# Performance work log

Measured on AMD Instinct MI355X. Metric: run time of the kernel, lower is better.

## Reference

```python
import jax, jax.numpy as jnp
import numpy as np

INPUT_SIZE = 64
HIDDEN_SIZE = 256
NUM_CLASSES = 10
BATCH = 512
SEQ_LEN = 1024


def setup_inputs() -> dict:
    key = jax.random.key(0)
    ks = jax.random.split(key, 6)
    std = 1.0 / np.sqrt(HIDDEN_SIZE)
    x = jax.random.normal(ks[0], (BATCH, SEQ_LEN, INPUT_SIZE), dtype=jnp.float32)
    # GRUCell params (reset_parameters: uniform(-std, std))
    Wx = jax.random.uniform(ks[1], (3 * HIDDEN_SIZE, INPUT_SIZE), minval=-std, maxval=std, dtype=jnp.float32)
    Wh = jax.random.uniform(ks[2], (3 * HIDDEN_SIZE, HIDDEN_SIZE), minval=-std, maxval=std, dtype=jnp.float32)
    bias = jax.random.uniform(ks[3], (3 * HIDDEN_SIZE,), minval=-std, maxval=std, dtype=jnp.float32)
    # fc: Linear(hidden_size, num_classes), default torch init ~ uniform(-1/sqrt(H), 1/sqrt(H))
    fc_w = jax.random.uniform(ks[4], (NUM_CLASSES, HIDDEN_SIZE), minval=-std, maxval=std, dtype=jnp.float32)
    fc_b = jax.random.uniform(ks[5], (NUM_CLASSES,), minval=-std, maxval=std, dtype=jnp.float32)
    return {"x": x, "Wx": Wx, "Wh": Wh, "bias": bias, "fc_w": fc_w, "fc_b": fc_b}


def reference(x, Wx, Wh, bias, fc_w, fc_b):
    B, S, _ = x.shape
    H = Wh.shape[1]
    b_r, b_z, b_h = jnp.split(bias, 3)
    # Precompute input gates for all timesteps in one GEMM: [B, S, 3H]
    gate_x = jnp.einsum('bsi,gi->bsg', x, Wx)

    def step(h, gx_t):
        gate_h = h @ Wh.T  # [B, 3H]
        i_r, i_z, i_h = jnp.split(gx_t, 3, axis=1)
        h_r, h_z, h_h = jnp.split(gate_h, 3, axis=1)
        reset_gate = jax.nn.sigmoid(i_r + h_r + b_r)
        update_gate = jax.nn.sigmoid(i_z + h_z + b_z)
        new_gate = jnp.tanh(i_h + reset_gate * h_h + b_h)
        hy = new_gate + update_gate * (h - new_gate)
        return hy, None

    h0 = jnp.zeros((B, H), dtype=x.dtype)
    hT, _ = jax.lax.scan(step, h0, jnp.swapaxes(gate_x, 0, 1))  # scan over time
    logit = hT @ fc_w.T + fc_b
    return logit
```

## Files before the change

kernel.cpp:

```cpp
#include <hip/hip_runtime.h>
#include <hip/hip_fp16.h>


typedef short v8s __attribute__((ext_vector_type(8)));
typedef float f32x4 __attribute__((ext_vector_type(4)));

#define LOG2E 1.4426950408889634f
#define GX_ELEMS (512ull * 1024ull * 768ull)
#define WS_NEED (GX_ELEMS * 2ull)

__device__ __forceinline__ unsigned short f2b(float f) {
    unsigned int u = __float_as_uint(f);
    u += 0x7FFFu + ((u >> 16) & 1u);
    return (unsigned short)(u >> 16);
}
__device__ __forceinline__ float b2f(unsigned short h) {
    return __uint_as_float(((unsigned int)h) << 16);
}
__device__ __forceinline__ v8s cvt8(f32x4 a, f32x4 b) {
    v8s r;
#pragma unroll
    for (int j = 0; j < 4; ++j) { r[j] = (short)f2b(a[j]); r[4 + j] = (short)f2b(b[j]); }
    return r;
}
__device__ __forceinline__ v8s wfrag(const float* src, float s) {
    f32x4 a = *(const f32x4*)src, b = *(const f32x4*)(src + 4);
    a *= s; b *= s;
    return cvt8(a, b);
}
__device__ __forceinline__ float rcpf(float v) {
#if __has_builtin(__builtin_amdgcn_rcpf)
    return __builtin_amdgcn_rcpf(v);
#else
    return 1.0f / v;
#endif
}
__device__ __forceinline__ float exp2f_(float v) {
#if __has_builtin(__builtin_amdgcn_exp2f)
    return __builtin_amdgcn_exp2f(v);
#else
    return __exp2f(v);
#endif
}
__device__ __forceinline__ float sg(float v) { return rcpf(1.0f + exp2f_(-v)); }
__device__ __forceinline__ float sigm(float v) {
    float e = __expf(-fmaxf(v, -30.0f));
    return rcpf(1.0f + e);
}
__device__ __forceinline__ float tanh_(float v) {
    float vc = fmaxf(fminf(v, 30.0f), -30.0f);
    float e = __expf(-2.0f * vc);
    return (1.0f - e) * rcpf(1.0f + e);
}
__device__ __forceinline__ f32x4 MF(v8s a, v8s b, f32x4 c) {
    return __builtin_amdgcn_mfma_f32_16x16x32_bf16(a, b, c, 0, 0, 0);
}
__device__ __forceinline__ int fidx(int row, int k) {
    return ((k >> 5) << 9) + ((((k >> 3) & 3) << 4) + row) * 8 + (k & 7);
}

extern "C" __global__ void __launch_bounds__(512)
gx_prepass(const float* __restrict__ x, const float* __restrict__ Wx,
           const float* __restrict__ bias, __half* __restrict__ gx)
{
    extern __shared__ char plds[];
    v8s* wxf = (v8s*)plds;

    const int tid = threadIdx.x;
    const int w = tid >> 6, l = tid & 63;
    const int cl = l & 15, kg = l >> 4;
    const int g = blockIdx.x & 31, tc = blockIdx.x >> 5;
    const int b0 = g << 4;

    for (int fid = w; fid < 96; fid += 8) {
        int ct = fid >> 1, k2 = fid & 1;
        float sc = (ct < 32) ? LOG2E : 2.0f * LOG2E;
        const float* src = Wx + (size_t)(ct * 16 + cl) * 64 + k2 * 32 + kg * 8;
        wxf[fid * 64 + l] = wfrag(src, sc);
    }
    __syncthreads();

    const int tiles[6] = {2*w, 2*w+1, 16+2*w, 17+2*w, 32+2*w, 33+2*w};
    float bv[6];
#pragma unroll
    for (int tt = 0; tt < 6; ++tt)
        bv[tt] = bias[tiles[tt] * 16 + cl] * ((tt < 4) ? LOG2E : 2.0f * LOG2E);

    for (int t16 = 0; t16 < 16; ++t16) {
        const int t = tc * 16 + t16;
        const float* xs = x + ((size_t)(b0 + cl) * 1024 + t) * 64 + kg * 8;
        v8s a0 = cvt8(*(const f32x4*)xs,        *(const f32x4*)(xs + 4));
        v8s a1 = cvt8(*(const f32x4*)(xs + 32), *(const f32x4*)(xs + 36));

        f32x4 acc[6];
#pragma unroll
        for (int tt = 0; tt < 6; ++tt) {
            acc[tt] = f32x4{0, 0, 0, 0};
            acc[tt] = MF(a0, wxf[(tiles[tt] * 2) * 64 + l], acc[tt]);
            acc[tt] = MF(a1, wxf[(tiles[tt] * 2 + 1) * 64 + l], acc[tt]);
        }
        const size_t rbase = (size_t)t * 512 + b0 + (kg << 2);
#pragma unroll
        for (int tt = 0; tt < 6; ++tt)
#pragma unroll
            for (int i = 0; i < 4; ++i)
                gx[(rbase + i) * 768 + tiles[tt] * 16 + cl] =
                    __float2half_rn(acc[tt][i] + bv[tt]);
    }
}

#define S_LDS_WHN  0
#define S_LDS_H    131072
#define S_LDS_SIZE 147456

extern "C" __global__ void __launch_bounds__(512, 2)
gru_scan2(const float* __restrict__ Wh, const __half* __restrict__ gx,
          const float* __restrict__ fcw, const float* __restrict__ fcb,
          float* __restrict__ out)
{
    extern __shared__ char lds[];
    v8s* whn = (v8s*)(lds + S_LDS_WHN);
    char* hl = lds + S_LDS_H;

    const int tid = threadIdx.x;
    const int w = tid >> 6, l = tid & 63;
    const int cl = l & 15, kg = l >> 4;
    const int b0 = blockIdx.x << 4;

    for (int f = w; f < 128; f += 8) {
        int t5 = f >> 3, ks = f & 7;
        const float* src = Wh + (size_t)(512 + t5 * 16 + cl) * 256 + ks * 32 + kg * 8;
        whn[f * 64 + l] = wfrag(src, 2.0f * LOG2E);
    }
    v8s whB[4][8];
#pragma unroll
    for (int tt = 0; tt < 4; ++tt) {
        const int tv = (tt < 2) ? (2 * w + tt) : (16 + 2 * w + (tt - 2));
        const float* src = Wh + (size_t)(tv * 16 + cl) * 256 + kg * 8;
#pragma unroll
        for (int ks = 0; ks < 8; ++ks)
            whB[tt][ks] = wfrag(src + ks * 32, LOG2E);
    }

    for (int i = tid; i < 2048; i += 512) ((unsigned int*)hl)[i] = 0u;
    float hprev[8] = {0, 0, 0, 0, 0, 0, 0, 0};
    const int wn0 = (2 * w) * 8, wn1 = (2 * w + 1) * 8;
    const __half* gq = gx + (size_t)(b0 + (kg << 2)) * 768 + w * 32 + cl;

    for (int t = 0; t < 1024; ++t) {
        __syncthreads();
        const int cur = t & 1;
        const v8s* hb = (const v8s*)(hl + cur * 8192);

        __half gxv[24];
#pragma unroll
        for (int gate = 0; gate < 3; ++gate)
#pragma unroll
            for (int p = 0; p < 2; ++p)
#pragma unroll
                for (int i = 0; i < 4; ++i)
                    gxv[gate * 8 + p * 4 + i] = gq[gate * 256 + p * 16 + i * 768];
        gq += 393216;

        f32x4 aR[2] = {{0,0,0,0},{0,0,0,0}}, aZ[2] = {{0,0,0,0},{0,0,0,0}},
              aN[2] = {{0,0,0,0},{0,0,0,0}};
#pragma unroll
        for (int ks = 0; ks < 8; ++ks) {
            v8s a  = hb[(ks << 6) + l];
            v8s n0 = whn[(wn0 + ks) * 64 + l];
            v8s n1 = whn[(wn1 + ks) * 64 + l];
            aR[0] = MF(a, whB[0][ks], aR[0]);
            aR[1] = MF(a, whB[1][ks], aR[1]);
            aZ[0] = MF(a, whB[2][ks], aZ[0]);
            aZ[1] = MF(a, whB[3][ks], aZ[1]);
            aN[0] = MF(a, n0, aN[0]);
            aN[1] = MF(a, n1, aN[1]);
        }

        unsigned short* hn = (unsigned short*)(hl + (cur ^ 1) * 8192);
#pragma unroll
        for (int p = 0; p < 2; ++p) {
            const int ch = w * 32 + p * 16 + cl;
            const int chbase = ((ch >> 5) << 9) + (((ch >> 3) & 3) << 7) + (ch & 7);
#pragma unroll
            for (int i = 0; i < 4; ++i) {
                float rg = sg(aR[p][i] + __half2float(gxv[p * 4 + i]));
                float zg = sg(aZ[p][i] + __half2float(gxv[8 + p * 4 + i]));
                float nv = __builtin_fmaf(rg, aN[p][i], __half2float(gxv[16 + p * 4 + i]));
                float ng = __builtin_fmaf(2.0f, sg(nv), -1.0f);
                float hy = ng + zg * (hprev[p * 4 + i] - ng);
                hprev[p * 4 + i] = hy;
                hn[chbase + ((kg << 2) + i) * 8] = f2b(hy);
            }
        }
    }

    __syncthreads();
    const unsigned short* hf = (const unsigned short*)hl;
    if (tid < 160) {
        int row = tid / 10, cls = tid - row * 10;
        float s = fcb[cls];
        const float* wrow = fcw + cls * 256;
        for (int k = 0; k < 256; ++k)
            s += b2f(hf[fidx(row, k)]) * wrow[k];
        out[(b0 + row) * 10 + cls] = s;
    }
}

#define FB_LDS_SIZE 151552
extern "C" __global__ void __launch_bounds__(512, 2)
gru_fb(const float* __restrict__ x, const float* __restrict__ Wx,
       const float* __restrict__ Wh, const float* __restrict__ bias,
       const float* __restrict__ fcw, const float* __restrict__ fcb,
       float* __restrict__ out)
{
    extern __shared__ char lds[];
    v8s* whn = (v8s*)lds;
    char* hl = lds + 131072;
    char* xl = lds + 147456;
    const int tid = threadIdx.x;
    const int w = tid >> 6, l = tid & 63;
    const int cl = l & 15, kg = l >> 4;
    const int b0 = blockIdx.x << 4;
    const int tiles[6] = {2*w, 2*w+1, 16+2*w, 17+2*w, 32+2*w, 33+2*w};

    for (int f = w; f < 128; f += 8) {
        int t5 = f >> 3, ks = f & 7;
        const float* src = Wh + (size_t)(512 + t5*16 + cl)*256 + ks*32 + kg*8;
        whn[f*64 + l] = wfrag(src, 1.0f);
    }
    v8s whB[4][8];
#pragma unroll
    for (int tt = 0; tt < 4; ++tt) {
        const float* src = Wh + (size_t)(tiles[tt]*16 + cl)*256 + kg*8;
#pragma unroll
        for (int ks = 0; ks < 8; ++ks)
            whB[tt][ks] = wfrag(src + ks*32, 1.0f);
    }
    float brv[2], bzv[2], bhv[2];
#pragma unroll
    for (int p = 0; p < 2; ++p) {
        int ch = (w << 5) + (p << 4) + cl;
        brv[p] = bias[ch]; bzv[p] = bias[256+ch]; bhv[p] = bias[512+ch];
    }
    for (int i = tid; i < 2048; i += 512) ((unsigned int*)hl)[i] = 0u;
    const int xr = tid >> 5, xc = (tid & 31) << 1;
    const int xidx = fidx(xr, xc);
    const float* xp = x + (((size_t)(b0 + xr)) << 16) + xc;
    {
        unsigned int pk = (unsigned int)f2b(xp[0]) | ((unsigned int)f2b(xp[1]) << 16);
        *(unsigned int*)(xl + xidx*2) = pk;
    }
    xp += 64;
    const int wn0 = (2*w)*8, wn1 = (2*w+1)*8;

    for (int t = 0; t < 1024; ++t) {
        __syncthreads();
        const int cur = t & 1;
        const v8s* hb = (const v8s*)(hl + cur*8192);
        const v8s* xb = (const v8s*)(xl + cur*2048);
        float xv0 = 0.0f, xv1 = 0.0f;
        if (t < 1023) { xv0 = xp[0]; xv1 = xp[1]; xp += 64; }
        v8s wxr[12];
#pragma unroll
        for (int tt = 0; tt < 6; ++tt) {
            const float* s0 = Wx + (size_t)(tiles[tt]*16 + cl)*64 + kg*8;
            wxr[tt*2]   = wfrag(s0, 1.0f);
            wxr[tt*2+1] = wfrag(s0 + 32, 1.0f);
        }
        f32x4 acc[8];
#pragma unroll
        for (int i = 0; i < 8; ++i) acc[i] = f32x4{0,0,0,0};
#pragma unroll
        for (int ks = 0; ks < 8; ++ks) {
            v8s a = hb[(ks << 6) + l];
            v8s n0 = whn[(wn0 + ks)*64 + l];
            v8s n1 = whn[(wn1 + ks)*64 + l];
            acc[0] = MF(a, whB[0][ks], acc[0]);
            acc[1] = MF(a, whB[1][ks], acc[1]);
            acc[2] = MF(a, whB[2][ks], acc[2]);
            acc[3] = MF(a, whB[3][ks], acc[3]);
            acc[4] = MF(a, n0, acc[4]);
            acc[5] = MF(a, n1, acc[5]);
        }
#pragma unroll
        for (int k2 = 0; k2 < 2; ++k2) {
            v8s ax = xb[(k2 << 6) + l];
            acc[0] = MF(ax, wxr[0+k2], acc[0]);
            acc[1] = MF(ax, wxr[2+k2], acc[1]);
            acc[2] = MF(ax, wxr[4+k2], acc[2]);
            acc[3] = MF(ax, wxr[6+k2], acc[3]);
            acc[6] = MF(ax, wxr[8+k2], acc[6]);
            acc[7] = MF(ax, wxr[10+k2], acc[7]);
        }
        const unsigned short* hc16 = (const unsigned short*)hb;
        unsigned short* hn16 = (unsigned short*)(hl + ((cur ^ 1) * 8192));
#pragma unroll
        for (int p = 0; p < 2; ++p) {
            int ch = (w << 5) + (p << 4) + cl;
            int chbase = ((ch >> 5) << 9) + (((ch >> 3) & 3) << 7) + (ch & 7);
#pragma unroll
            for (int i = 0; i < 4; ++i) {
                int row = (kg << 2) + i;
                int idx = chbase + (row << 3);
                float rg = sigm(acc[p][i] + brv[p]);
                float zg = sigm(acc[2+p][i] + bzv[p]);
                float ng = tanh_(acc[6+p][i] + bhv[p] + rg * acc[4+p][i]);
                float hold = b2f(hc16[idx]);
                float hy = ng + zg * (hold - ng);
                hn16[idx] = f2b(hy);
            }
        }
        if (t < 1023) {
            unsigned int pk = (unsigned int)f2b(xv0) | ((unsigned int)f2b(xv1) << 16);
            *(unsigned int*)(xl + ((cur ^ 1) * 2048) + xidx*2) = pk;
        }
    }
    __syncthreads();
    const unsigned short* hf = (const unsigned short*)hl;
    if (tid < 160) {
        int row = tid / 10, cls = tid - row * 10;
        float s = fcb[cls];
        const float* wrow = fcw + cls * 256;
        for (int k = 0; k < 256; ++k)
            s += b2f(hf[fidx(row, k)]) * wrow[k];
        out[(b0 + row)*10 + cls] = s;
    }
}

extern "C" void kernel_launch(void* const* d_in, const int* in_sizes, int n_in,
                              void* d_out, int out_size, void* d_ws, size_t ws_size,
                              hipStream_t stream) {
    const float* x    = (const float*)d_in[0];
    const float* Wx   = (const float*)d_in[1];
    const float* Wh   = (const float*)d_in[2];
    const float* bias = (const float*)d_in[3];
    const float* fcw  = (const float*)d_in[4];
    const float* fcb  = (const float*)d_in[5];

    if (ws_size >= WS_NEED) {
        (void)hipFuncSetAttribute((const void*)gx_prepass,
                                  hipFuncAttributeMaxDynamicSharedMemorySize, 98304);
        (void)hipFuncSetAttribute((const void*)gru_scan2,
                                  hipFuncAttributeMaxDynamicSharedMemorySize, S_LDS_SIZE);
        gx_prepass<<<dim3(2048), dim3(512), 98304, stream>>>(
            x, Wx, bias, (__half*)d_ws);
        gru_scan2<<<dim3(32), dim3(512), S_LDS_SIZE, stream>>>(
            Wh, (const __half*)d_ws, fcw, fcb, (float*)d_out);
    } else {
        (void)hipFuncSetAttribute((const void*)gru_fb,
                                  hipFuncAttributeMaxDynamicSharedMemorySize, FB_LDS_SIZE);
        gru_fb<<<dim3(32), dim3(512), FB_LDS_SIZE, stream>>>(
            x, Wx, Wh, bias, fcw, fcb, (float*)d_out);
    }
}
```

Before: 2.029 ms.

## Fuse input-gate prepass into scan kernel with producer-consumer chunked ring buffer

```diff
diff --git a/kernel.cpp b/kernel.cpp
--- a/kernel.cpp
+++ b/kernel.cpp
@@ -4,10 +4,9 @@
 
 typedef short v8s __attribute__((ext_vector_type(8)));
 typedef float f32x4 __attribute__((ext_vector_type(4)));
+typedef unsigned short u16x4 __attribute__((ext_vector_type(4)));
 
 #define LOG2E 1.4426950408889634f
-#define GX_ELEMS (512ull * 1024ull * 768ull)
-#define WS_NEED (GX_ELEMS * 2ull)
 
 __device__ __forceinline__ unsigned short f2b(float f) {
     unsigned int u = __float_as_uint(f);
@@ -16,6 +15,16 @@
 }
 __device__ __forceinline__ float b2f(unsigned short h) {
     return __uint_as_float(((unsigned int)h) << 16);
+}
+__device__ __forceinline__ unsigned short f2h(float f) {
+    union { __half h; unsigned short u; } cv;
+    cv.h = __float2half_rn(f);
+    return cv.u;
+}
+__device__ __forceinline__ float h2f(unsigned short u) {
+    union { unsigned short u; __half h; } cv;
+    cv.u = u;
+    return __half2float(cv.h);
 }
 __device__ __forceinline__ v8s cvt8(f32x4 a, f32x4 b) {
     v8s r;
@@ -59,73 +68,93 @@
     return ((k >> 5) << 9) + ((((k >> 3) & 3) << 4) + row) * 8 + (k & 7);
 }
 
-extern "C" __global__ void __launch_bounds__(512)
-gx_prepass(const float* __restrict__ x, const float* __restrict__ Wx,
-           const float* __restrict__ bias, __half* __restrict__ gx)
+#define S_LDS_SIZE 147456
+
+extern "C" __global__ void __launch_bounds__(512, 2)
+gru_fused(const float* __restrict__ x, const float* __restrict__ Wx,
+          const float* __restrict__ Wh, const float* __restrict__ bias,
+          const float* __restrict__ fcw, const float* __restrict__ fcb,
+          unsigned short* __restrict__ gx, unsigned int* __restrict__ ctrl,
+          int n_slots, int ch_shift, float* __restrict__ out)
 {
-    extern __shared__ char plds[];
-    v8s* wxf = (v8s*)plds;
-
+    extern __shared__ char lds[];
     const int tid = threadIdx.x;
     const int w = tid >> 6, l = tid & 63;
     const int cl = l & 15, kg = l >> 4;
-    const int g = blockIdx.x & 31, tc = blockIdx.x >> 5;
-    const int b0 = g << 4;
-
-    for (int fid = w; fid < 96; fid += 8) {
-        int ct = fid >> 1, k2 = fid & 1;
-        float sc = (ct < 32) ? LOG2E : 2.0f * LOG2E;
-        const float* src = Wx + (size_t)(ct * 16 + cl) * 64 + k2 * 32 + kg * 8;
-        wxf[fid * 64 + l] = wfrag(src, sc);
-    }
-    __syncthreads();
-
-    const int tiles[6] = {2*w, 2*w+1, 16+2*w, 17+2*w, 32+2*w, 33+2*w};
-    float bv[6];
-#pragma unroll
-    for (int tt = 0; tt < 6; ++tt)
-        bv[tt] = bias[tiles[tt] * 16 + cl] * ((tt < 4) ? LOG2E : 2.0f * LOG2E);
-
-    for (int t16 = 0; t16 < 16; ++t16) {
-        const int t = tc * 16 + t16;
-        const float* xs = x + ((size_t)(b0 + cl) * 1024 + t) * 64 + kg * 8;
-        v8s a0 = cvt8(*(const f32x4*)xs,        *(const f32x4*)(xs + 4));
-        v8s a1 = cvt8(*(const f32x4*)(xs + 32), *(const f32x4*)(xs + 36));
-
-        f32x4 acc[6];
-#pragma unroll
-        for (int tt = 0; tt < 6; ++tt) {
-            acc[tt] = f32x4{0, 0, 0, 0};
-            acc[tt] = MF(a0, wxf[(tiles[tt] * 2) * 64 + l], acc[tt]);
-            acc[tt] = MF(a1, wxf[(tiles[tt] * 2 + 1) * 64 + l], acc[tt]);
-        }
-        const size_t rbase = (size_t)t * 512 + b0 + (kg << 2);
+    const size_t slot_elems = 393216ull << ch_shift;
+
+    if (blockIdx.x >= 32) {
+        v8s* wxf = (v8s*)lds;
+        const int pid = blockIdx.x - 32;
+        const int cs4 = ch_shift - 4;
+
+        for (int fid = w; fid < 96; fid += 8) {
+            int ct = fid >> 1, k2 = fid & 1;
+            float sc = (ct < 32) ? LOG2E : 2.0f * LOG2E;
+            const float* src = Wx + (size_t)(ct * 16 + cl) * 64 + k2 * 32 + kg * 8;
+            wxf[fid * 64 + l] = wfrag(src, sc);
+        }
+        const int tiles[6] = {2*w, 2*w+1, 16+2*w, 17+2*w, 32+2*w, 33+2*w};
+        float bv[6];
 #pragma unroll
         for (int tt = 0; tt < 6; ++tt)
-#pragma unroll
-            for (int i = 0; i < 4; ++i)
-                gx[(rbase + i) * 768 + tiles[tt] * 16 + cl] =
-                    __float2half_rn(acc[tt][i] + bv[tt]);
-    }
-}
-
-#define S_LDS_WHN  0
-#define S_LDS_H    131072
-#define S_LDS_SIZE 147456
-
-extern "C" __global__ void __launch_bounds__(512, 2)
-gru_scan2(const float* __restrict__ Wh, const __half* __restrict__ gx,
-          const float* __restrict__ fcw, const float* __restrict__ fcb,
-          float* __restrict__ out)
-{
-    extern __shared__ char lds[];
-    v8s* whn = (v8s*)(lds + S_LDS_WHN);
-    char* hl = lds + S_LDS_H;
-
-    const int tid = threadIdx.x;
-    const int w = tid >> 6, l = tid & 63;
-    const int cl = l & 15, kg = l >> 4;
+            bv[tt] = bias[tiles[tt] * 16 + cl] * ((tt < 4) ? LOG2E : 2.0f * LOG2E);
+        __syncthreads();
+
+        for (int j = pid; j < 2048; j += 224) {
+            const int tc = j >> 5, g = j & 31;
+            const int c = tc >> cs4;
+            const int b0 = g << 4;
+            if (c >= n_slots) {
+                if (tid == 0) {
+                    while (__hip_atomic_load(&ctrl[64 + (c - n_slots)],
+                                             __ATOMIC_ACQUIRE,
+                                             __HIP_MEMORY_SCOPE_AGENT) < 32u)
+                        __builtin_amdgcn_s_sleep(16);
+                }
+                __syncthreads();
+            }
+            unsigned short* gs = gx + (size_t)(c % n_slots) * slot_elems;
+            const int tl0 = (tc << 4) - (c << ch_shift);
+
+            for (int t16 = 0; t16 < 16; ++t16) {
+                const int t = (tc << 4) + t16;
+                const int tl = tl0 + t16;
+                const float* xs = x + ((size_t)(b0 + cl) * 1024 + t) * 64 + kg * 8;
+                v8s a0 = cvt8(*(const f32x4*)xs,        *(const f32x4*)(xs + 4));
+                v8s a1 = cvt8(*(const f32x4*)(xs + 32), *(const f32x4*)(xs + 36));
+
+                f32x4 acc[6];
+#pragma unroll
+                for (int tt = 0; tt < 6; ++tt) {
+                    acc[tt] = f32x4{0, 0, 0, 0};
+                    acc[tt] = MF(a0, wxf[(tiles[tt] * 2) * 64 + l], acc[tt]);
+                    acc[tt] = MF(a1, wxf[(tiles[tt] * 2 + 1) * 64 + l], acc[tt]);
+                }
+#pragma unroll
+                for (int tt = 0; tt < 6; ++tt) {
+                    u16x4 pk;
+#pragma unroll
+                    for (int i = 0; i < 4; ++i)
+                        pk[i] = f2h(acc[tt][i] + bv[tt]);
+                    *(u16x4*)(gs + (size_t)(tl * 768 + tiles[tt] * 16 + cl) * 512
+                                 + b0 + (kg << 2)) = pk;
+                }
+            }
+            __syncthreads();
+            if (tid == 0)
+                __hip_atomic_fetch_add(&ctrl[c], 1u, __ATOMIC_RELEASE,
+                                       __HIP_MEMORY_SCOPE_AGENT);
+        }
+        return;
+    }
+
+    v8s* whn = (v8s*)lds;
+    char* hl = lds + 131072;
     const int b0 = blockIdx.x << 4;
+    const int nchunk = 1024 >> ch_shift;
+    const int chs = 1 << ch_shift;
+    const unsigned int jobs_pc = 32u << (ch_shift - 4);
 
     for (int f = w; f < 128; f += 8) {
         int t5 = f >> 3, ks = f & 7;
@@ -141,58 +170,69 @@
         for (int ks = 0; ks < 8; ++ks)
             whB[tt][ks] = wfrag(src + ks * 32, LOG2E);
     }
-
     for (int i = tid; i < 2048; i += 512) ((unsigned int*)hl)[i] = 0u;
     float hprev[8] = {0, 0, 0, 0, 0, 0, 0, 0};
     const int wn0 = (2 * w) * 8, wn1 = (2 * w + 1) * 8;
-    const __half* gq = gx + (size_t)(b0 + (kg << 2)) * 768 + w * 32 + cl;
-
-    for (int t = 0; t < 1024; ++t) {
+    const size_t gxoff = (size_t)((w << 5) + cl) * 512 + b0 + (kg << 2);
+
+    int t = 0;
+    for (int c = 0; c < nchunk; ++c) {
+        if (tid == 0) {
+            while (__hip_atomic_load(&ctrl[c], __ATOMIC_ACQUIRE,
+                                     __HIP_MEMORY_SCOPE_AGENT) < jobs_pc)
+                __builtin_amdgcn_s_sleep(16);
+        }
+        const unsigned short* gp = gx + (size_t)(c % n_slots) * slot_elems + gxoff;
+
+        for (int t2 = 0; t2 < chs; ++t2, ++t) {
+            __syncthreads();
+            const int cur = t & 1;
+            const v8s* hb = (const v8s*)(hl + cur * 8192);
+
+            u16x4 gv[6];
+#pragma unroll
+            for (int gi = 0; gi < 3; ++gi)
+#pragma unroll
+                for (int p = 0; p < 2; ++p)
+                    gv[gi * 2 + p] = *(const u16x4*)(gp + (size_t)(gi * 256 + p * 16) * 512);
+            gp += 393216;
+
+            f32x4 aR[2] = {{0,0,0,0},{0,0,0,0}}, aZ[2] = {{0,0,0,0},{0,0,0,0}},
+                  aN[2] = {{0,0,0,0},{0,0,0,0}};
+#pragma unroll
+            for (int ks = 0; ks < 8; ++ks) {
+                v8s a  = hb[(ks << 6) + l];
+                v8s n0 = whn[(wn0 + ks) * 64 + l];
+                v8s n1 = whn[(wn1 + ks) * 64 + l];
+                aR[0] = MF(a, whB[0][ks], aR[0]);
+                aR[1] = MF(a, whB[1][ks], aR[1]);
+                aZ[0] = MF(a, whB[2][ks], aZ[0]);
+                aZ[1] = MF(a, whB[3][ks], aZ[1]);
+                aN[0] = MF(a, n0, aN[0]);
+                aN[1] = MF(a, n1, aN[1]);
+            }
+
+            unsigned short* hn = (unsigned short*)(hl + (cur ^ 1) * 8192);
+#pragma unroll
+            for (int p = 0; p < 2; ++p) {
+                const int ch = (w << 5) + (p << 4) + cl;
+                const int chbase = ((ch >> 5) << 9) + (((ch >> 3) & 3) << 7) + (ch & 7);
+#pragma unroll
+                for (int i = 0; i < 4; ++i) {
+                    float rg = sg(aR[p][i] + h2f(gv[p][i]));
+                    float zg = sg(aZ[p][i] + h2f(gv[2 + p][i]));
+                    float nv = __builtin_fmaf(rg, aN[p][i], h2f(gv[4 + p][i]));
+                    float ng = __builtin_fmaf(2.0f, sg(nv), -1.0f);
+                    float hy = ng + zg * (hprev[p * 4 + i] - ng);
+                    hprev[p * 4 + i] = hy;
+                    hn[chbase + ((kg << 2) + i) * 8] = f2b(hy);
+                }
+            }
+        }
         __syncthreads();
-        const int cur = t & 1;
-        const v8s* hb = (const v8s*)(hl + cur * 8192);
-
-        __half gxv[24];
-#pragma unroll
-        for (int gate = 0; gate < 3; ++gate)
-#pragma unroll
-            for (int p = 0; p < 2; ++p)
-#pragma unroll
-                for (int i = 0; i < 4; ++i)
-                    gxv[gate * 8 + p * 4 + i] = gq[gate * 256 + p * 16 + i * 768];
-        gq += 393216;
-
-        f32x4 aR[2] = {{0,0,0,0},{0,0,0,0}}, aZ[2] = {{0,0,0,0},{0,0,0,0}},
-              aN[2] = {{0,0,0,0},{0,0,0,0}};
-#pragma unroll
-        for (int ks = 0; ks < 8; ++ks) {
-            v8s a  = hb[(ks << 6) + l];
-            v8s n0 = whn[(wn0 + ks) * 64 + l];
-            v8s n1 = whn[(wn1 + ks) * 64 + l];
-            aR[0] = MF(a, whB[0][ks], aR[0]);
-            aR[1] = MF(a, whB[1][ks], aR[1]);
-            aZ[0] = MF(a, whB[2][ks], aZ[0]);
-            aZ[1] = MF(a, whB[3][ks], aZ[1]);
-            aN[0] = MF(a, n0, aN[0]);
-            aN[1] = MF(a, n1, aN[1]);
-        }
-
-        unsigned short* hn = (unsigned short*)(hl + (cur ^ 1) * 8192);
-#pragma unroll
-        for (int p = 0; p < 2; ++p) {
-            const int ch = w * 32 + p * 16 + cl;
-            const int chbase = ((ch >> 5) << 9) + (((ch >> 3) & 3) << 7) + (ch & 7);
-#pragma unroll
-            for (int i = 0; i < 4; ++i) {
-                float rg = sg(aR[p][i] + __half2float(gxv[p * 4 + i]));
-                float zg = sg(aZ[p][i] + __half2float(gxv[8 + p * 4 + i]));
-                float nv = __builtin_fmaf(rg, aN[p][i], __half2float(gxv[16 + p * 4 + i]));
-                float ng = __builtin_fmaf(2.0f, sg(nv), -1.0f);
-                float hy = ng + zg * (hprev[p * 4 + i] - ng);
-                hprev[p * 4 + i] = hy;
-                hn[chbase + ((kg << 2) + i) * 8] = f2b(hy);
-            }
-        }
+        if (tid == 0)
+            __hip_atomic_fetch_add(&ctrl[64 + c], 1u, __ATOMIC_RELEASE,
+                                   __HIP_MEMORY_SCOPE_AGENT);
     }
 
     __syncthreads();
@@ -338,15 +378,26 @@
     const float* fcw  = (const float*)d_in[4];
     const float* fcb  = (const float*)d_in[5];
 
-    if (ws_size >= WS_NEED) {
-        (void)hipFuncSetAttribute((const void*)gx_prepass,
-                                  hipFuncAttributeMaxDynamicSharedMemorySize, 98304);
-        (void)hipFuncSetAttribute((const void*)gru_scan2,
+    int ch_shift = -1, n_slots = 0;
+    for (int cs = 6; cs >= 4; --cs) {
+        unsigned long long slot = 786432ull << cs;
+        if (ws_size < 1024ull + 2ull * slot) continue;
+        int nch = 1024 >> cs;
+        unsigned long long n = (ws_size - 1024ull) / slot;
+        n_slots = (n > (unsigned long long)nch) ? nch : (int)n;
+        ch_shift = cs;
+        break;
+    }
+
+    if (ch_shift >= 4) {
+        unsigned int* ctrl =
+            (unsigned int*)((char*)d_ws + (786432ull << ch_shift) * (size_t)n_slots);
+        (void)hipMemsetAsync(ctrl, 0, 1024, stream);
+        (void)hipFuncSetAttribute((const void*)gru_fused,
                                   hipFuncAttributeMaxDynamicSharedMemorySize, S_LDS_SIZE);
-        gx_prepass<<<dim3(2048), dim3(512), 98304, stream>>>(
-            x, Wx, bias, (__half*)d_ws);
-        gru_scan2<<<dim3(32), dim3(512), S_LDS_SIZE, stream>>>(
-            Wh, (const __half*)d_ws, fcw, fcb, (float*)d_out);
+        gru_fused<<<dim3(256), dim3(512), S_LDS_SIZE, stream>>>(
+            x, Wx, Wh, bias, fcw, fcb,
+            (unsigned short*)d_ws, ctrl, n_slots, ch_shift, (float*)d_out);
     } else {
         (void)hipFuncSetAttribute((const void*)gru_fb,
                                   hipFuncAttributeMaxDynamicSharedMemorySize, FB_LDS_SIZE);
```

After: 6.118 ms. 3.01x slower.

## Fuse input projection into recurrent scan and drop the gx prepass

Applied to the files above, without the earlier changes.

```diff
diff --git a/kernel.cpp b/kernel.cpp
--- a/kernel.cpp
+++ b/kernel.cpp
@@ -1,13 +1,10 @@
 #include <hip/hip_runtime.h>
-#include <hip/hip_fp16.h>
 
 
 typedef short v8s __attribute__((ext_vector_type(8)));
 typedef float f32x4 __attribute__((ext_vector_type(4)));
 
 #define LOG2E 1.4426950408889634f
-#define GX_ELEMS (512ull * 1024ull * 768ull)
-#define WS_NEED (GX_ELEMS * 2ull)
 
 __device__ __forceinline__ unsigned short f2b(float f) {
     unsigned int u = __float_as_uint(f);
@@ -43,15 +40,6 @@
 #endif
 }
 __device__ __forceinline__ float sg(float v) { return rcpf(1.0f + exp2f_(-v)); }
-__device__ __forceinline__ float sigm(float v) {
-    float e = __expf(-fmaxf(v, -30.0f));
-    return rcpf(1.0f + e);
-}
-__device__ __forceinline__ float tanh_(float v) {
-    float vc = fmaxf(fminf(v, 30.0f), -30.0f);
-    float e = __expf(-2.0f * vc);
-    return (1.0f - e) * rcpf(1.0f + e);
-}
 __device__ __forceinline__ f32x4 MF(v8s a, v8s b, f32x4 c) {
     return __builtin_amdgcn_mfma_f32_16x16x32_bf16(a, b, c, 0, 0, 0);
 }
@@ -59,165 +47,21 @@
     return ((k >> 5) << 9) + ((((k >> 3) & 3) << 4) + row) * 8 + (k & 7);
 }
 
-extern "C" __global__ void __launch_bounds__(512)
-gx_prepass(const float* __restrict__ x, const float* __restrict__ Wx,
-           const float* __restrict__ bias, __half* __restrict__ gx)
-{
-    extern __shared__ char plds[];
-    v8s* wxf = (v8s*)plds;
-
-    const int tid = threadIdx.x;
-    const int w = tid >> 6, l = tid & 63;
-    const int cl = l & 15, kg = l >> 4;
-    const int g = blockIdx.x & 31, tc = blockIdx.x >> 5;
-    const int b0 = g << 4;
-
-    for (int fid = w; fid < 96; fid += 8) {
-        int ct = fid >> 1, k2 = fid & 1;
-        float sc = (ct < 32) ? LOG2E : 2.0f * LOG2E;
-        const float* src = Wx + (size_t)(ct * 16 + cl) * 64 + k2 * 32 + kg * 8;
-        wxf[fid * 64 + l] = wfrag(src, sc);
-    }
-    __syncthreads();
-
-    const int tiles[6] = {2*w, 2*w+1, 16+2*w, 17+2*w, 32+2*w, 33+2*w};
-    float bv[6];
-#pragma unroll
-    for (int tt = 0; tt < 6; ++tt)
-        bv[tt] = bias[tiles[tt] * 16 + cl] * ((tt < 4) ? LOG2E : 2.0f * LOG2E);
-
-    for (int t16 = 0; t16 < 16; ++t16) {
-        const int t = tc * 16 + t16;
-        const float* xs = x + ((size_t)(b0 + cl) * 1024 + t) * 64 + kg * 8;
-        v8s a0 = cvt8(*(const f32x4*)xs,        *(const f32x4*)(xs + 4));
-        v8s a1 = cvt8(*(const f32x4*)(xs + 32), *(const f32x4*)(xs + 36));
-
-        f32x4 acc[6];
-#pragma unroll
-        for (int tt = 0; tt < 6; ++tt) {
-            acc[tt] = f32x4{0, 0, 0, 0};
-            acc[tt] = MF(a0, wxf[(tiles[tt] * 2) * 64 + l], acc[tt]);
-            acc[tt] = MF(a1, wxf[(tiles[tt] * 2 + 1) * 64 + l], acc[tt]);
-        }
-        const size_t rbase = (size_t)t * 512 + b0 + (kg << 2);
-#pragma unroll
-        for (int tt = 0; tt < 6; ++tt)
-#pragma unroll
-            for (int i = 0; i < 4; ++i)
-                gx[(rbase + i) * 768 + tiles[tt] * 16 + cl] =
-                    __float2half_rn(acc[tt][i] + bv[tt]);
-    }
-}
-
-#define S_LDS_WHN  0
-#define S_LDS_H    131072
-#define S_LDS_SIZE 147456
+#define LDS_H    131072
+#define LDS_X    147456
+#define LDS_SIZE 151552
 
 extern "C" __global__ void __launch_bounds__(512, 2)
-gru_scan2(const float* __restrict__ Wh, const __half* __restrict__ gx,
-          const float* __restrict__ fcw, const float* __restrict__ fcb,
-          float* __restrict__ out)
-{
-    extern __shared__ char lds[];
-    v8s* whn = (v8s*)(lds + S_LDS_WHN);
-    char* hl = lds + S_LDS_H;
-
-    const int tid = threadIdx.x;
-    const int w = tid >> 6, l = tid & 63;
-    const int cl = l & 15, kg = l >> 4;
-    const int b0 = blockIdx.x << 4;
-
-    for (int f = w; f < 128; f += 8) {
-        int t5 = f >> 3, ks = f & 7;
-        const float* src = Wh + (size_t)(512 + t5 * 16 + cl) * 256 + ks * 32 + kg * 8;
-        whn[f * 64 + l] = wfrag(src, 2.0f * LOG2E);
-    }
-    v8s whB[4][8];
-#pragma unroll
-    for (int tt = 0; tt < 4; ++tt) {
-        const int tv = (tt < 2) ? (2 * w + tt) : (16 + 2 * w + (tt - 2));
-        const float* src = Wh + (size_t)(tv * 16 + cl) * 256 + kg * 8;
-#pragma unroll
-        for (int ks = 0; ks < 8; ++ks)
-            whB[tt][ks] = wfrag(src + ks * 32, LOG2E);
-    }
-
-    for (int i = tid; i < 2048; i += 512) ((unsigned int*)hl)[i] = 0u;
-    float hprev[8] = {0, 0, 0, 0, 0, 0, 0, 0};
-    const int wn0 = (2 * w) * 8, wn1 = (2 * w + 1) * 8;
-    const __half* gq = gx + (size_t)(b0 + (kg << 2)) * 768 + w * 32 + cl;
-
-    for (int t = 0; t < 1024; ++t) {
-        __syncthreads();
-        const int cur = t & 1;
-        const v8s* hb = (const v8s*)(hl + cur * 8192);
-
-        __half gxv[24];
-#pragma unroll
-        for (int gate = 0; gate < 3; ++gate)
-#pragma unroll
-            for (int p = 0; p < 2; ++p)
-#pragma unroll
-                for (int i = 0; i < 4; ++i)
-                    gxv[gate * 8 + p * 4 + i] = gq[gate * 256 + p * 16 + i * 768];
-        gq += 393216;
-
-        f32x4 aR[2] = {{0,0,0,0},{0,0,0,0}}, aZ[2] = {{0,0,0,0},{0,0,0,0}},
-              aN[2] = {{0,0,0,0},{0,0,0,0}};
-#pragma unroll
-        for (int ks = 0; ks < 8; ++ks) {
-            v8s a  = hb[(ks << 6) + l];
-            v8s n0 = whn[(wn0 + ks) * 64 + l];
-            v8s n1 = whn[(wn1 + ks) * 64 + l];
-            aR[0] = MF(a, whB[0][ks], aR[0]);
-            aR[1] = MF(a, whB[1][ks], aR[1]);
-            aZ[0] = MF(a, whB[2][ks], aZ[0]);
-            aZ[1] = MF(a, whB[3][ks], aZ[1]);
-            aN[0] = MF(a, n0, aN[0]);
-            aN[1] = MF(a, n1, aN[1]);
-        }
-
-        unsigned short* hn = (unsigned short*)(hl + (cur ^ 1) * 8192);
-#pragma unroll
-        for (int p = 0; p < 2; ++p) {
-            const int ch = w * 32 + p * 16 + cl;
-            const int chbase = ((ch >> 5) << 9) + (((ch >> 3) & 3) << 7) + (ch & 7);
-#pragma unroll
-            for (int i = 0; i < 4; ++i) {
-                float rg = sg(aR[p][i] + __half2float(gxv[p * 4 + i]));
-                float zg = sg(aZ[p][i] + __half2float(gxv[8 + p * 4 + i]));
-                float nv = __builtin_fmaf(rg, aN[p][i], __half2float(gxv[16 + p * 4 + i]));
-                float ng = __builtin_fmaf(2.0f, sg(nv), -1.0f);
-                float hy = ng + zg * (hprev[p * 4 + i] - ng);
-                hprev[p * 4 + i] = hy;
-                hn[chbase + ((kg << 2) + i) * 8] = f2b(hy);
-            }
-        }
-    }
-
-    __syncthreads();
-    const unsigned short* hf = (const unsigned short*)hl;
-    if (tid < 160) {
-        int row = tid / 10, cls = tid - row * 10;
-        float s = fcb[cls];
-        const float* wrow = fcw + cls * 256;
-        for (int k = 0; k < 256; ++k)
-            s += b2f(hf[fidx(row, k)]) * wrow[k];
-        out[(b0 + row) * 10 + cls] = s;
-    }
-}
-
-#define FB_LDS_SIZE 151552
-extern "C" __global__ void __launch_bounds__(512, 2)
-gru_fb(const float* __restrict__ x, const float* __restrict__ Wx,
+gru_v7(const float* __restrict__ x, const float* __restrict__ Wx,
        const float* __restrict__ Wh, const float* __restrict__ bias,
        const float* __restrict__ fcw, const float* __restrict__ fcb,
        float* __restrict__ out)
 {
     extern __shared__ char lds[];
     v8s* whn = (v8s*)lds;
-    char* hl = lds + 131072;
-    char* xl = lds + 147456;
+    char* hl = lds + LDS_H;
+    char* xl = lds + LDS_X;
+
     const int tid = threadIdx.x;
     const int w = tid >> 6, l = tid & 63;
     const int cl = l & 15, kg = l >> 4;
@@ -227,7 +71,7 @@
     for (int f = w; f < 128; f += 8) {
         int t5 = f >> 3, ks = f & 7;
         const float* src = Wh + (size_t)(512 + t5*16 + cl)*256 + ks*32 + kg*8;
-        whn[f*64 + l] = wfrag(src, 1.0f);
+        whn[f*64 + l] = wfrag(src, 2.0f*LOG2E);
     }
     v8s whB[4][8];
 #pragma unroll
@@ -235,15 +79,28 @@
         const float* src = Wh + (size_t)(tiles[tt]*16 + cl)*256 + kg*8;
 #pragma unroll
         for (int ks = 0; ks < 8; ++ks)
-            whB[tt][ks] = wfrag(src + ks*32, 1.0f);
+            whB[tt][ks] = wfrag(src + ks*32, LOG2E);
+    }
+    v8s wxr[12];
+#pragma unroll
+    for (int tt = 0; tt < 6; ++tt) {
+        const float sc = (tt < 4) ? LOG2E : 2.0f*LOG2E;
+        const float* s0 = Wx + (size_t)(tiles[tt]*16 + cl)*64 + kg*8;
+        wxr[tt*2]   = wfrag(s0, sc);
+        wxr[tt*2+1] = wfrag(s0 + 32, sc);
     }
     float brv[2], bzv[2], bhv[2];
 #pragma unroll
     for (int p = 0; p < 2; ++p) {
         int ch = (w << 5) + (p << 4) + cl;
-        brv[p] = bias[ch]; bzv[p] = bias[256+ch]; bhv[p] = bias[512+ch];
-    }
+        brv[p] = bias[ch] * LOG2E;
+        bzv[p] = bias[256 + ch] * LOG2E;
+        bhv[p] = bias[512 + ch] * 2.0f*LOG2E;
+    }
+
     for (int i = tid; i < 2048; i += 512) ((unsigned int*)hl)[i] = 0u;
+    float hprev[8] = {0, 0, 0, 0, 0, 0, 0, 0};
+
     const int xr = tid >> 5, xc = (tid & 31) << 1;
     const int xidx = fidx(xr, xc);
     const float* xp = x + (((size_t)(b0 + xr)) << 16) + xc;
@@ -259,21 +116,23 @@
         const int cur = t & 1;
         const v8s* hb = (const v8s*)(hl + cur*8192);
         const v8s* xb = (const v8s*)(xl + cur*2048);
+
         float xv0 = 0.0f, xv1 = 0.0f;
         if (t < 1023) { xv0 = xp[0]; xv1 = xp[1]; xp += 64; }
-        v8s wxr[12];
-#pragma unroll
-        for (int tt = 0; tt < 6; ++tt) {
-            const float* s0 = Wx + (size_t)(tiles[tt]*16 + cl)*64 + kg*8;
-            wxr[tt*2]   = wfrag(s0, 1.0f);
-            wxr[tt*2+1] = wfrag(s0 + 32, 1.0f);
-        }
+
         f32x4 acc[8];
-#pragma unroll
-        for (int i = 0; i < 8; ++i) acc[i] = f32x4{0,0,0,0};
+        acc[0] = f32x4{brv[0], brv[0], brv[0], brv[0]};
+        acc[1] = f32x4{brv[1], brv[1], brv[1], brv[1]};
+        acc[2] = f32x4{bzv[0], bzv[0], bzv[0], bzv[0]};
+        acc[3] = f32x4{bzv[1], bzv[1], bzv[1], bzv[1]};
+        acc[4] = f32x4{0, 0, 0, 0};
+        acc[5] = f32x4{0, 0, 0, 0};
+        acc[6] = f32x4{bhv[0], bhv[0], bhv[0], bhv[0]};
+        acc[7] = f32x4{bhv[1], bhv[1], bhv[1], bhv[1]};
+
 #pragma unroll
         for (int ks = 0; ks < 8; ++ks) {
-            v8s a = hb[(ks << 6) + l];
+            v8s a  = hb[(ks << 6) + l];
             v8s n0 = whn[(wn0 + ks)*64 + l];
             v8s n1 = whn[(wn1 + ks)*64 + l];
             acc[0] = MF(a, whB[0][ks], acc[0]);
@@ -286,29 +145,28 @@
 #pragma unroll
         for (int k2 = 0; k2 < 2; ++k2) {
             v8s ax = xb[(k2 << 6) + l];
-            acc[0] = MF(ax, wxr[0+k2], acc[0]);
-            acc[1] = MF(ax, wxr[2+k2], acc[1]);
-            acc[2] = MF(ax, wxr[4+k2], acc[2]);
-            acc[3] = MF(ax, wxr[6+k2], acc[3]);
-            acc[6] = MF(ax, wxr[8+k2], acc[6]);
-            acc[7] = MF(ax, wxr[10+k2], acc[7]);
-        }
-        const unsigned short* hc16 = (const unsigned short*)hb;
-        unsigned short* hn16 = (unsigned short*)(hl + ((cur ^ 1) * 8192));
+            acc[0] = MF(ax, wxr[0  + k2], acc[0]);
+            acc[1] = MF(ax, wxr[2  + k2], acc[1]);
+            acc[2] = MF(ax, wxr[4  + k2], acc[2]);
+            acc[3] = MF(ax, wxr[6  + k2], acc[3]);
+            acc[6] = MF(ax, wxr[8  + k2], acc[6]);
+            acc[7] = MF(ax, wxr[10 + k2], acc[7]);
+        }
+
+        unsigned short* hn = (unsigned short*)(hl + (cur ^ 1) * 8192);
 #pragma unroll
         for (int p = 0; p < 2; ++p) {
-            int ch = (w << 5) + (p << 4) + cl;
-            int chbase = ((ch >> 5) << 9) + (((ch >> 3) & 3) << 7) + (ch & 7);
+            const int ch = (w << 5) + (p << 4) + cl;
+            const int chbase = ((ch >> 5) << 9) + (((ch >> 3) & 3) << 7) + (ch & 7);
 #pragma unroll
             for (int i = 0; i < 4; ++i) {
-                int row = (kg << 2) + i;
-                int idx = chbase + (row << 3);
-                float rg = sigm(acc[p][i] + brv[p]);
-                float zg = sigm(acc[2+p][i] + bzv[p]);
-                float ng = tanh_(acc[6+p][i] + bhv[p] + rg * acc[4+p][i]);
-                float hold = b2f(hc16[idx]);
-                float hy = ng + zg * (hold - ng);
-                hn16[idx] = f2b(hy);
+                float rg = sg(acc[p][i]);
+                float zg = sg(acc[2 + p][i]);
+                float nv = __builtin_fmaf(rg, acc[4 + p][i], acc[6 + p][i]);
+                float ng = __builtin_fmaf(2.0f, sg(nv), -1.0f);
+                float hy = ng + zg * (hprev[p*4 + i] - ng);
+                hprev[p*4 + i] = hy;
+                hn[chbase + ((kg << 2) + i) * 8] = f2b(hy);
             }
         }
         if (t < 1023) {
@@ -316,6 +174,7 @@
             *(unsigned int*)(xl + ((cur ^ 1) * 2048) + xidx*2) = pk;
         }
     }
+
     __syncthreads();
     const unsigned short* hf = (const unsigned short*)hl;
     if (tid < 160) {
@@ -337,20 +196,10 @@
     const float* bias = (const float*)d_in[3];
     const float* fcw  = (const float*)d_in[4];
     const float* fcb  = (const float*)d_in[5];
-
-    if (ws_size >= WS_NEED) {
-        (void)hipFuncSetAttribute((const void*)gx_prepass,
-                                  hipFuncAttributeMaxDynamicSharedMemorySize, 98304);
-        (void)hipFuncSetAttribute((const void*)gru_scan2,
-                                  hipFuncAttributeMaxDynamicSharedMemorySize, S_LDS_SIZE);
-        gx_prepass<<<dim3(2048), dim3(512), 98304, stream>>>(
-            x, Wx, bias, (__half*)d_ws);
-        gru_scan2<<<dim3(32), dim3(512), S_LDS_SIZE, stream>>>(
-            Wh, (const __half*)d_ws, fcw, fcb, (float*)d_out);
-    } else {
-        (void)hipFuncSetAttribute((const void*)gru_fb,
-                                  hipFuncAttributeMaxDynamicSharedMemorySize, FB_LDS_SIZE);
-        gru_fb<<<dim3(32), dim3(512), FB_LDS_SIZE, stream>>>(
-            x, Wx, Wh, bias, fcw, fcb, (float*)d_out);
-    }
-}
+    (void)d_ws; (void)ws_size;
+
+    (void)hipFuncSetAttribute((const void*)gru_v7,
+                              hipFuncAttributeMaxDynamicSharedMemorySize, LDS_SIZE);
+    gru_v7<<<dim3(32), dim3(512), LDS_SIZE, stream>>>(
+        x, Wx, Wh, bias, fcw, fcb, (float*)d_out);
+}
```

New measurement: 1.967 ms. -3.1%, faster.

## Fuse input-gate GEMM into scan kernel with per-chunk workspace staging

Applied to the files above, without the earlier changes.

```diff
diff --git a/kernel.cpp b/kernel.cpp
--- a/kernel.cpp
+++ b/kernel.cpp
@@ -4,10 +4,13 @@
 
 typedef short v8s __attribute__((ext_vector_type(8)));
 typedef float f32x4 __attribute__((ext_vector_type(4)));
+typedef unsigned int u32x4 __attribute__((ext_vector_type(4)));
+typedef unsigned int u32x2 __attribute__((ext_vector_type(2)));
 
 #define LOG2E 1.4426950408889634f
-#define GX_ELEMS (512ull * 1024ull * 768ull)
-#define WS_NEED (GX_ELEMS * 2ull)
+#define CHUNK 32
+#define NCHUNK 32
+#define WS_NEED (32ull * CHUNK * 24576ull)
 
 __device__ __forceinline__ unsigned short f2b(float f) {
     unsigned int u = __float_as_uint(f);
@@ -16,6 +19,13 @@
 }
 __device__ __forceinline__ float b2f(unsigned short h) {
     return __uint_as_float(((unsigned int)h) << 16);
+}
+__device__ __forceinline__ unsigned short f2h(float f) {
+    return __half_as_ushort(__float2half_rn(f));
+}
+__device__ __forceinline__ float hxu(unsigned int u, int hi) {
+    unsigned short b = (unsigned short)(hi ? (u >> 16) : (u & 0xFFFFu));
+    return __half2float(__ushort_as_half(b));
 }
 __device__ __forceinline__ v8s cvt8(f32x4 a, f32x4 b) {
     v8s r;
@@ -59,138 +69,153 @@
     return ((k >> 5) << 9) + ((((k >> 3) & 3) << 4) + row) * 8 + (k & 7);
 }
 
-extern "C" __global__ void __launch_bounds__(512)
-gx_prepass(const float* __restrict__ x, const float* __restrict__ Wx,
-           const float* __restrict__ bias, __half* __restrict__ gx)
-{
-    extern __shared__ char plds[];
-    v8s* wxf = (v8s*)plds;
-
-    const int tid = threadIdx.x;
-    const int w = tid >> 6, l = tid & 63;
-    const int cl = l & 15, kg = l >> 4;
-    const int g = blockIdx.x & 31, tc = blockIdx.x >> 5;
-    const int b0 = g << 4;
-
-    for (int fid = w; fid < 96; fid += 8) {
-        int ct = fid >> 1, k2 = fid & 1;
-        float sc = (ct < 32) ? LOG2E : 2.0f * LOG2E;
-        const float* src = Wx + (size_t)(ct * 16 + cl) * 64 + k2 * 32 + kg * 8;
-        wxf[fid * 64 + l] = wfrag(src, sc);
-    }
-    __syncthreads();
-
-    const int tiles[6] = {2*w, 2*w+1, 16+2*w, 17+2*w, 32+2*w, 33+2*w};
-    float bv[6];
-#pragma unroll
-    for (int tt = 0; tt < 6; ++tt)
-        bv[tt] = bias[tiles[tt] * 16 + cl] * ((tt < 4) ? LOG2E : 2.0f * LOG2E);
-
-    for (int t16 = 0; t16 < 16; ++t16) {
-        const int t = tc * 16 + t16;
-        const float* xs = x + ((size_t)(b0 + cl) * 1024 + t) * 64 + kg * 8;
-        v8s a0 = cvt8(*(const f32x4*)xs,        *(const f32x4*)(xs + 4));
-        v8s a1 = cvt8(*(const f32x4*)(xs + 32), *(const f32x4*)(xs + 36));
-
-        f32x4 acc[6];
-#pragma unroll
-        for (int tt = 0; tt < 6; ++tt) {
-            acc[tt] = f32x4{0, 0, 0, 0};
-            acc[tt] = MF(a0, wxf[(tiles[tt] * 2) * 64 + l], acc[tt]);
-            acc[tt] = MF(a1, wxf[(tiles[tt] * 2 + 1) * 64 + l], acc[tt]);
-        }
-        const size_t rbase = (size_t)t * 512 + b0 + (kg << 2);
-#pragma unroll
-        for (int tt = 0; tt < 6; ++tt)
-#pragma unroll
-            for (int i = 0; i < 4; ++i)
-                gx[(rbase + i) * 768 + tiles[tt] * 16 + cl] =
-                    __float2half_rn(acc[tt][i] + bv[tt]);
-    }
-}
-
-#define S_LDS_WHN  0
-#define S_LDS_H    131072
-#define S_LDS_SIZE 147456
+#define LDS8_X    16384
+#define LDS8_SIZE 81920
 
 extern "C" __global__ void __launch_bounds__(512, 2)
-gru_scan2(const float* __restrict__ Wh, const __half* __restrict__ gx,
-          const float* __restrict__ fcw, const float* __restrict__ fcb,
-          float* __restrict__ out)
+gru_v8(const float* __restrict__ x, const float* __restrict__ Wx,
+       const float* __restrict__ Wh, const float* __restrict__ bias,
+       const float* __restrict__ fcw, const float* __restrict__ fcb,
+       unsigned short* __restrict__ ws, float* __restrict__ out)
 {
     extern __shared__ char lds[];
-    v8s* whn = (v8s*)(lds + S_LDS_WHN);
-    char* hl = lds + S_LDS_H;
+    char* hl = lds;
+    char* xf = lds + LDS8_X;
 
     const int tid = threadIdx.x;
     const int w = tid >> 6, l = tid & 63;
     const int cl = l & 15, kg = l >> 4;
     const int b0 = blockIdx.x << 4;
-
-    for (int f = w; f < 128; f += 8) {
-        int t5 = f >> 3, ks = f & 7;
-        const float* src = Wh + (size_t)(512 + t5 * 16 + cl) * 256 + ks * 32 + kg * 8;
-        whn[f * 64 + l] = wfrag(src, 2.0f * LOG2E);
-    }
+    const int tiles[6] = {2*w, 2*w+1, 16+2*w, 17+2*w, 32+2*w, 33+2*w};
+
     v8s whB[4][8];
 #pragma unroll
     for (int tt = 0; tt < 4; ++tt) {
-        const int tv = (tt < 2) ? (2 * w + tt) : (16 + 2 * w + (tt - 2));
-        const float* src = Wh + (size_t)(tv * 16 + cl) * 256 + kg * 8;
+        const float* src = Wh + (size_t)(tiles[tt]*16 + cl)*256 + kg*8;
 #pragma unroll
         for (int ks = 0; ks < 8; ++ks)
-            whB[tt][ks] = wfrag(src + ks * 32, LOG2E);
+            whB[tt][ks] = wfrag(src + ks*32, LOG2E);
     }
 
     for (int i = tid; i < 2048; i += 512) ((unsigned int*)hl)[i] = 0u;
     float hprev[8] = {0, 0, 0, 0, 0, 0, 0, 0};
-    const int wn0 = (2 * w) * 8, wn1 = (2 * w + 1) * 8;
-    const __half* gq = gx + (size_t)(b0 + (kg << 2)) * 768 + w * 32 + cl;
-
-    for (int t = 0; t < 1024; ++t) {
+
+    unsigned short* gxb = ws + (size_t)blockIdx.x * (CHUNK * 12288);
+
+    const int tl_x  = tid >> 4;
+    const int k0    = (tid & 15) << 2;
+    const int k2x   = k0 >> 5;
+    const int laned = ((k0 & 31) >> 3) << 4;
+    const int e2    = (k0 & 7) << 1;
+    char* const xfd = xf + (tl_x*2 + k2x)*1024 + e2;
+
+    for (int c = 0; c < NCHUNK; ++c) {
+        const int c0 = c << 5;
         __syncthreads();
-        const int cur = t & 1;
-        const v8s* hb = (const v8s*)(hl + cur * 8192);
-
-        __half gxv[24];
-#pragma unroll
-        for (int gate = 0; gate < 3; ++gate)
-#pragma unroll
-            for (int p = 0; p < 2; ++p)
-#pragma unroll
-                for (int i = 0; i < 4; ++i)
-                    gxv[gate * 8 + p * 4 + i] = gq[gate * 256 + p * 16 + i * 768];
-        gq += 393216;
-
-        f32x4 aR[2] = {{0,0,0,0},{0,0,0,0}}, aZ[2] = {{0,0,0,0},{0,0,0,0}},
-              aN[2] = {{0,0,0,0},{0,0,0,0}};
-#pragma unroll
-        for (int ks = 0; ks < 8; ++ks) {
-            v8s a  = hb[(ks << 6) + l];
-            v8s n0 = whn[(wn0 + ks) * 64 + l];
-            v8s n1 = whn[(wn1 + ks) * 64 + l];
-            aR[0] = MF(a, whB[0][ks], aR[0]);
-            aR[1] = MF(a, whB[1][ks], aR[1]);
-            aZ[0] = MF(a, whB[2][ks], aZ[0]);
-            aZ[1] = MF(a, whB[3][ks], aZ[1]);
-            aN[0] = MF(a, n0, aN[0]);
-            aN[1] = MF(a, n1, aN[1]);
-        }
-
-        unsigned short* hn = (unsigned short*)(hl + (cur ^ 1) * 8192);
-#pragma unroll
-        for (int p = 0; p < 2; ++p) {
-            const int ch = w * 32 + p * 16 + cl;
-            const int chbase = ((ch >> 5) << 9) + (((ch >> 3) & 3) << 7) + (ch & 7);
-#pragma unroll
-            for (int i = 0; i < 4; ++i) {
-                float rg = sg(aR[p][i] + __half2float(gxv[p * 4 + i]));
-                float zg = sg(aZ[p][i] + __half2float(gxv[8 + p * 4 + i]));
-                float nv = __builtin_fmaf(rg, aN[p][i], __half2float(gxv[16 + p * 4 + i]));
-                float ng = __builtin_fmaf(2.0f, sg(nv), -1.0f);
-                float hy = ng + zg * (hprev[p * 4 + i] - ng);
-                hprev[p * 4 + i] = hy;
-                hn[chbase + ((kg << 2) + i) * 8] = f2b(hy);
+
+#pragma unroll
+        for (int r = 0; r < 16; ++r) {
+            f32x4 v = *(const f32x4*)(x + ((size_t)(b0 + r) << 16)
+                                        + (c0 << 6) + (tid << 2));
+            unsigned int p0 = (unsigned int)f2b(v[0]) | ((unsigned int)f2b(v[1]) << 16);
+            unsigned int p1 = (unsigned int)f2b(v[2]) | ((unsigned int)f2b(v[3]) << 16);
+            u32x2 pk = {p0, p1};
+            *(u32x2*)(xfd + (laned + r)*16) = pk;
+        }
+        __syncthreads();
+
+        {
+            v8s wxr[12];
+            float bv[6];
+#pragma unroll
+            for (int tt = 0; tt < 6; ++tt) {
+                const float sc = (tt < 4) ? LOG2E : 2.0f*LOG2E;
+                const float* s0 = Wx + (size_t)(tiles[tt]*16 + cl)*64 + kg*8;
+                wxr[tt*2]   = wfrag(s0, sc);
+                wxr[tt*2+1] = wfrag(s0 + 32, sc);
+                bv[tt] = bias[tiles[tt]*16 + cl] * sc;
+            }
+            const v8s* xv = (const v8s*)xf;
+            unsigned int* gp = (unsigned int*)(gxb + (size_t)((w << 6) + l) * 24);
+            for (int tl = 0; tl < CHUNK; ++tl) {
+                v8s a0 = xv[(tl*2)*64 + l];
+                v8s a1 = xv[(tl*2+1)*64 + l];
+                f32x4 acc[6];
+#pragma unroll
+                for (int tt = 0; tt < 6; ++tt)
+                    acc[tt] = f32x4{bv[tt], bv[tt], bv[tt], bv[tt]};
+#pragma unroll
+                for (int tt = 0; tt < 6; ++tt) {
+                    acc[tt] = MF(a0, wxr[tt*2],   acc[tt]);
+                    acc[tt] = MF(a1, wxr[tt*2+1], acc[tt]);
+                }
+                unsigned int q[12];
+#pragma unroll
+                for (int tt = 0; tt < 6; ++tt) {
+                    q[tt*2]   = (unsigned int)f2h(acc[tt][0]) | ((unsigned int)f2h(acc[tt][1]) << 16);
+                    q[tt*2+1] = (unsigned int)f2h(acc[tt][2]) | ((unsigned int)f2h(acc[tt][3]) << 16);
+                }
+                u32x4 s0 = {q[0], q[1], q[2],  q[3]};
+                u32x4 s1 = {q[4], q[5], q[6],  q[7]};
+                u32x4 s2 = {q[8], q[9], q[10], q[11]};
+                *(u32x4*)(gp)     = s0;
+                *(u32x4*)(gp + 4) = s1;
+                *(u32x4*)(gp + 8) = s2;
+                gp += 12 * 512;
+            }
+        }
+        __syncthreads();
+
+        {
+            v8s whN[2][8];
+#pragma unroll
+            for (int j = 0; j < 2; ++j) {
+                const float* src = Wh + (size_t)(512 + (2*w + j)*16 + cl)*256 + kg*8;
+#pragma unroll
+                for (int ks = 0; ks < 8; ++ks)
+                    whN[j][ks] = wfrag(src + ks*32, 2.0f*LOG2E);
+            }
+            const unsigned short* gq0 = gxb + (size_t)((w << 6) + l) * 24;
+            for (int tl = 0; tl < CHUNK; ++tl) {
+                const int t = c0 + tl;
+                __syncthreads();
+                const int cur = t & 1;
+                const v8s* hb = (const v8s*)(hl + cur * 8192);
+
+                const u32x4* gq = (const u32x4*)(gq0 + (size_t)tl * 12288);
+                u32x4 gr = gq[0], gz = gq[1], gn = gq[2];
+
+                f32x4 aR[2] = {{0,0,0,0},{0,0,0,0}},
+                      aZ[2] = {{0,0,0,0},{0,0,0,0}},
+                      aN[2] = {{0,0,0,0},{0,0,0,0}};
+#pragma unroll
+                for (int ks = 0; ks < 8; ++ks) {
+                    v8s a = hb[(ks << 6) + l];
+                    aR[0] = MF(a, whB[0][ks], aR[0]);
+                    aR[1] = MF(a, whB[1][ks], aR[1]);
+                    aZ[0] = MF(a, whB[2][ks], aZ[0]);
+                    aZ[1] = MF(a, whB[3][ks], aZ[1]);
+                    aN[0] = MF(a, whN[0][ks], aN[0]);
+                    aN[1] = MF(a, whN[1][ks], aN[1]);
+                }
+
+                unsigned short* hn = (unsigned short*)(hl + (cur ^ 1) * 8192);
+#pragma unroll
+                for (int p = 0; p < 2; ++p) {
+                    const int ch = (w << 5) + (p << 4) + cl;
+                    const int chbase = ((ch >> 5) << 9) + (((ch >> 3) & 3) << 7) + (ch & 7);
+#pragma unroll
+                    for (int i = 0; i < 4; ++i) {
+                        const int dw = p*2 + (i >> 1), hi = i & 1;
+                        float rg = sg(aR[p][i] + hxu(gr[dw], hi));
+                        float zg = sg(aZ[p][i] + hxu(gz[dw], hi));
+                        float nv = __builtin_fmaf(rg, aN[p][i], hxu(gn[dw], hi));
+                        float ng = __builtin_fmaf(2.0f, sg(nv), -1.0f);
+                        float hy = ng + zg * (hprev[p*4 + i] - ng);
+                        hprev[p*4 + i] = hy;
+                        hn[chbase + ((kg << 2) + i) * 8] = f2b(hy);
+                    }
+                }
             }
         }
     }
@@ -339,14 +364,10 @@
     const float* fcb  = (const float*)d_in[5];
 
     if (ws_size >= WS_NEED) {
-        (void)hipFuncSetAttribute((const void*)gx_prepass,
-                                  hipFuncAttributeMaxDynamicSharedMemorySize, 98304);
-        (void)hipFuncSetAttribute((const void*)gru_scan2,
-                                  hipFuncAttributeMaxDynamicSharedMemorySize, S_LDS_SIZE);
-        gx_prepass<<<dim3(2048), dim3(512), 98304, stream>>>(
-            x, Wx, bias, (__half*)d_ws);
-        gru_scan2<<<dim3(32), dim3(512), S_LDS_SIZE, stream>>>(
-            Wh, (const __half*)d_ws, fcw, fcb, (float*)d_out);
+        (void)hipFuncSetAttribute((const void*)gru_v8,
+                                  hipFuncAttributeMaxDynamicSharedMemorySize, LDS8_SIZE);
+        gru_v8<<<dim3(32), dim3(512), LDS8_SIZE, stream>>>(
+            x, Wx, Wh, bias, fcw, fcb, (unsigned short*)d_ws, (float*)d_out);
     } else {
         (void)hipFuncSetAttribute((const void*)gru_fb,
                                   hipFuncAttributeMaxDynamicSharedMemorySize, FB_LDS_SIZE);
```

Result: slower. 2.885 ms (+42.2%).
